# Kernel tuning notes

Measured on AMD Instinct MI355X. Metric: run time of the kernel, lower is better.

## Reference

```python
import jax, jax.numpy as jnp
import numpy as np

TAPS = 5
DELAY = 3
ITERATIONS = 2
EPS = 1e-10


def wpe_one_iteration(Y, power, taps=TAPS, delay=DELAY, eps=EPS):
    """One WPE iteration.
    Y: (B, F, C, T) complex STFT signal.
    power: (B, F, T) real power estimate.
    Returns dereverberated signal, same shape as Y.
    """
    B, F, C, T = Y.shape
    inv_pow = 1.0 / jnp.maximum(power, eps)  # (B,F,T)

    # Tap-delayed (Toeplitz-like) stacked signal: Ytil[..., p, d, t] = Y[..., d, t - delay - p]
    Ytil = jnp.stack(
        [jnp.pad(Y[..., : T - delay - p], ((0, 0), (0, 0), (0, 0), (delay + p, 0)))
         for p in range(taps)],
        axis=2,
    )  # (B, F, taps, C, T)

    # Original implementation only accumulates statistics for frames where the
    # full tap window is available: t >= delay + taps - 1.
    valid = (jnp.arange(T) >= delay + taps - 1).astype(power.dtype)
    w = inv_pow * valid  # (B,F,T)

    Psi_w = jnp.conj(Ytil) * w[:, :, None, None, :]  # (B,F,taps,C,T)

    # Power-weighted covariance matrix R[(p,d),(q,e)] and cross-correlation b[(p,d),e]
    R = jnp.einsum('bfpdt,bfqet->bfpdqe', Psi_w, Ytil).reshape(B, F, taps * C, taps * C)
    b = jnp.einsum('bfpdt,bfet->bfpde', Psi_w, Y).reshape(B, F, taps * C, C)

    eye = jnp.eye(taps * C, dtype=R.dtype)
    # Batched per-frequency linear solve for the conjugate filter matrix
    G_conj = jnp.linalg.solve(R + eps * eye, b).reshape(B, F, taps, C, C)

    # reverb tail: sum over taps p and source channels d
    reverb_tail = jnp.einsum('bfpde,bfpdt->bfet', G_conj, Ytil)
    return Y - reverb_tail


def setup_inputs() -> dict:
    key = jax.random.key(0)
    k1, k2 = jax.random.split(key)
    B, T, C, F = 8, 512, 8, 257
    data_real = jax.random.normal(k1, (B, T, C, F), dtype=jnp.float32)
    data_imag = jax.random.normal(k2, (B, T, C, F), dtype=jnp.float32)
    ilens = jnp.full((B,), T, dtype=jnp.int64)
    return {"data_real": data_real, "data_imag": data_imag, "ilens": ilens}


def reference(data_real, data_imag, ilens):
    # data: (B, T, C, F) -> (B, F, C, T)
    data = (data_real + 1j * data_imag).astype(jnp.complex64)
    Y = jnp.transpose(data, (0, 3, 2, 1))  # (B,F,C,T)
    enhanced = Y
    for _ in range(ITERATIONS):
        power = jnp.mean(enhanced.real ** 2 + enhanced.imag ** 2, axis=-2)  # (B,F,T)
        enhanced = wpe_one_iteration(Y, power)
        # NOTE: original code calls `enhanced.masked_fill(...)` (non in-place),
        # whose result is discarded -> it is a no-op; ilens here are all == T anyway.
    enhanced = jnp.transpose(enhanced, (0, 3, 2, 1))  # (B,T,C,F)
    # Return real/imag stacked so output is a real float tensor (B,T,C,F,2)
    return jnp.stack([enhanced.real, enhanced.imag], axis=-1)
```

## Files before the change

### kernel.cpp

```cpp
#include <hip/hip_runtime.h>

constexpr int BB = 8;
constexpr int TT = 512;
constexpr int CHN = 8;
constexpr int FF = 257;
constexpr int TAPS = 5;
constexpr int DELAY = 3;
constexpr int NBF = BB * FF;
constexpr int ROWQ = 20;
constexpr int MC = 48;
constexpr int RS = 98;

typedef short s8v __attribute__((ext_vector_type(8)));
typedef float f4  __attribute__((ext_vector_type(4)));

__global__ void k_pack(const float* __restrict__ re, const float* __restrict__ im,
                       float* __restrict__ Yg, float* __restrict__ pw) {
  const int ft = blockIdx.x, tt = blockIdx.y, b = blockIdx.z;
  const int f0 = ft * 32, t0 = tt * 16;
  __shared__ float ls[32 * 258];
  const int tid = threadIdx.x;
  const int l = tid & 31;
  const int r = tid >> 5;
  const int f = f0 + l;
  if (f < FF) {
    for (int k = 0; k < 32; ++k) {
      const int task = r + 8 * k;
      const int ri = task & 1;
      const int c  = (task >> 1) & 7;
      const int t  = task >> 4;
      const float* src = ri ? im : re;
      const float v = src[(((size_t)b * TT + t0 + t) * CHN + c) * FF + f];
      ls[l * 258 + (t * 16 + c * 2 + ri)] = v;
    }
  }
  __syncthreads();
  for (int ff = 0; ff < 32; ++ff) {
    const int fg = f0 + ff;
    if (fg >= FF) break;
    Yg[(((size_t)b * FF + fg) * TT + t0) * 16 + tid] = ls[ff * 258 + tid];
  }
  if (f < FF) {
#pragma unroll
    for (int s = 0; s < 2; ++s) {
      const int t = (tid >> 5) + 8 * s;
      const float* row = &ls[l * 258 + t * 16];
      float ss = 0.f;
#pragma unroll
      for (int q = 0; q < 8; ++q) {
        const float2 v = *(const float2*)&row[q * 2];
        ss += v.x * v.x + v.y * v.y;
      }
      pw[((size_t)b * FF + f) * TT + t0 + t] = ss * (1.0f / CHN);
    }
  }
}

__device__ __forceinline__ unsigned bf16rn(float x) {
  unsigned b = __float_as_uint(x);
  return (b + 0x7fffu + ((b >> 16) & 1u)) >> 16;
}

__global__ __launch_bounds__(384, 4)
void k_corr(const float* __restrict__ Yg,
            const float* __restrict__ pw,
            float2* __restrict__ Mg) {
  const int bf = blockIdx.x;
  __shared__ float pre[512 * 9];
  __shared__ float pim[512 * 9];
  __shared__ unsigned short tiles[4 * 1920];
  const int tid = threadIdx.x;

  for (int t = tid; t < TT; t += 384) {
    const float p = pw[(size_t)bf * TT + t];
    pre[t * 9 + 8] = (t >= DELAY + TAPS - 1) ? rsqrtf(fmaxf(p, 1e-10f)) : 0.0f;
  }
  const float4* ybase4 = (const float4*)(Yg + (size_t)bf * TT * 16);
  for (int fi = tid; fi < TT * 4; fi += 384) {
    const int t = fi >> 2, q = fi & 3;
    const float4 v = ybase4[fi];
    pre[t * 9 + 2 * q] = v.x; pre[t * 9 + 2 * q + 1] = v.z;
    pim[t * 9 + 2 * q] = v.y; pim[t * 9 + 2 * q + 1] = v.w;
  }
  __syncthreads();

  const int lane = tid & 63, wv = tid >> 6;
  const int rt = (wv < 3) ? 0 : (wv < 5 ? 1 : 2);
  const int ct = (wv < 3) ? wv : (wv < 5 ? wv - 2 : 2);
  const int lr = lane & 15, lk = lane >> 4;
  const int aoff = (rt * 16 + lr) * 40 + lk * 8;
  const int boff = (ct * 16 + lr) * 40 + lk * 8;

  f4 accre  = {0.f, 0.f, 0.f, 0.f};
  f4 accim1 = {0.f, 0.f, 0.f, 0.f};
  f4 accim2 = {0.f, 0.f, 0.f, 0.f};

  for (int kt = 0; kt < 16; ++kt) {
    const int kt0 = kt * 32;
#pragma unroll
    for (int cc = 0; cc < 2; ++cc) {
      const int c = tid + cc * 384;
      const int kp = c & 15, row = c >> 4;
      const int t = kt0 + 2 * kp;
      const int sh = (row < 40) ? (DELAY + (row >> 3)) : 0;
      const int e  = (row < 40) ? (row & 7) : (row - 40);
      int s0 = t - sh;     if (s0 < 0) s0 = 0;
      int s1 = t + 1 - sh; if (s1 < 0) s1 = 0;
      const float u0 = pre[t * 9 + 8], u1 = pre[(t + 1) * 9 + 8];
      const float v0r = u0 * pre[s0 * 9 + e], v0i = u0 * pim[s0 * 9 + e];
      const float v1r = u1 * pre[s1 * 9 + e], v1i = u1 * pim[s1 * 9 + e];
      const int idx = row * 40 + 2 * kp;
      {
        const unsigned b0 = __float_as_uint(v0r), b1 = __float_as_uint(v1r);
        *(unsigned*)&tiles[idx] = (b0 >> 16) | (b1 & 0xffff0000u);
        *(unsigned*)&tiles[1920 + idx] =
            bf16rn(v0r - __uint_as_float(b0 & 0xffff0000u)) |
            (bf16rn(v1r - __uint_as_float(b1 & 0xffff0000u)) << 16);
      }
      {
        const unsigned b0 = __float_as_uint(v0i), b1 = __float_as_uint(v1i);
        *(unsigned*)&tiles[3840 + idx] = (b0 >> 16) | (b1 & 0xffff0000u);
        *(unsigned*)&tiles[5760 + idx] =
            bf16rn(v0i - __uint_as_float(b0 & 0xffff0000u)) |
            (bf16rn(v1i - __uint_as_float(b1 & 0xffff0000u)) << 16);
      }
    }
    __syncthreads();
    const s8v crhA = *(const s8v*)&tiles[aoff];
    const s8v crlA = *(const s8v*)&tiles[1920 + aoff];
    const s8v cihA = *(const s8v*)&tiles[3840 + aoff];
    const s8v cilA = *(const s8v*)&tiles[5760 + aoff];
    const s8v crhB = *(const s8v*)&tiles[boff];
    const s8v crlB = *(const s8v*)&tiles[1920 + boff];
    const s8v cihB = *(const s8v*)&tiles[3840 + boff];
    const s8v cilB = *(const s8v*)&tiles[5760 + boff];
    accre  = __builtin_amdgcn_mfma_f32_16x16x32_bf16(crhA, crhB, accre, 0, 0, 0);
    accre  = __builtin_amdgcn_mfma_f32_16x16x32_bf16(crlA, crhB, accre, 0, 0, 0);
    accre  = __builtin_amdgcn_mfma_f32_16x16x32_bf16(crhA, crlB, accre, 0, 0, 0);
    accre  = __builtin_amdgcn_mfma_f32_16x16x32_bf16(cihA, cihB, accre, 0, 0, 0);
    accre  = __builtin_amdgcn_mfma_f32_16x16x32_bf16(cilA, cihB, accre, 0, 0, 0);
    accre  = __builtin_amdgcn_mfma_f32_16x16x32_bf16(cihA, cilB, accre, 0, 0, 0);
    accim1 = __builtin_amdgcn_mfma_f32_16x16x32_bf16(crhA, cihB, accim1, 0, 0, 0);
    accim1 = __builtin_amdgcn_mfma_f32_16x16x32_bf16(crlA, cihB, accim1, 0, 0, 0);
    accim1 = __builtin_amdgcn_mfma_f32_16x16x32_bf16(crhA, cilB, accim1, 0, 0, 0);
    accim2 = __builtin_amdgcn_mfma_f32_16x16x32_bf16(cihA, crhB, accim2, 0, 0, 0);
    accim2 = __builtin_amdgcn_mfma_f32_16x16x32_bf16(cilA, crhB, accim2, 0, 0, 0);
    accim2 = __builtin_amdgcn_mfma_f32_16x16x32_bf16(cihA, crlB, accim2, 0, 0, 0);
    __syncthreads();
  }

#pragma unroll
  for (int r = 0; r < 4; ++r) {
    const int i = rt * 16 + lk * 4 + r;
    const int j = ct * 16 + lr;
    const float revl = accre[r];
    const float imvl = accim1[r] - accim2[r];
    if (i < 40) {
      float rr = revl;
      if (i == j) rr += 1e-10f;
      Mg[((size_t)bf * 40 + i) * MC + j] = make_float2(rr, imvl);
    }
    if (rt < ct && j < 40) {
      Mg[((size_t)bf * 40 + j) * MC + i] = make_float2(revl, -imvl);
    }
  }
}

__global__ __launch_bounds__(128) void k_solve(const float2* __restrict__ Mg,
                                               float2* __restrict__ Gg) {
  const int bf = blockIdx.x;
  __shared__ float ml[40 * RS];
  const int tid = threadIdx.x;
  for (int idx = tid; idx < 40 * MC; idx += 128) {
    const int i = idx / MC, j = idx - i * MC;
    float2 v = Mg[((size_t)bf * 40 + i) * MC + j];
    *(float2*)&ml[i * RS + j * 2] = v;
  }
  __syncthreads();
  const int li = tid >> 3, lj = tid & 7;
  for (int k = 0; k < 40; ++k) {
    const float2 pv = *(float2*)&ml[k * RS + k * 2];
    const float den = pv.x * pv.x + pv.y * pv.y;
    const float inr = pv.x / den, ini = -pv.y / den;
    for (int i = k + 1 + li; i < 40; i += 16) {
      const float2 aik = *(float2*)&ml[i * RS + k * 2];
      const float fr = aik.x * inr - aik.y * ini;
      const float fi = aik.x * ini + aik.y * inr;
      for (int j = k + 1 + lj; j < MC; j += 8) {
        const float2 ak = *(float2*)&ml[k * RS + j * 2];
        float2 ai = *(float2*)&ml[i * RS + j * 2];
        ai.x -= fr * ak.x - fi * ak.y;
        ai.y -= fr * ak.y + fi * ak.x;
        *(float2*)&ml[i * RS + j * 2] = ai;
      }
    }
    __syncthreads();
  }
  const int lane = tid & 63, wave = tid >> 6;
  const int e = 4 * wave + (lane & 3), cc = lane >> 2;
  for (int k = 39; k >= 0; --k) {
    float sr = 0.f, si = 0.f;
    for (int j = k + 1 + cc; j < 40; j += 16) {
      const float2 u = *(float2*)&ml[k * RS + j * 2];
      const float2 x = *(float2*)&ml[j * RS + (40 + e) * 2];
      sr += u.x * x.x - u.y * x.y;
      si += u.x * x.y + u.y * x.x;
    }
    sr += __shfl_xor(sr, 4);  si += __shfl_xor(si, 4);
    sr += __shfl_xor(sr, 8);  si += __shfl_xor(si, 8);
    sr += __shfl_xor(sr, 16); si += __shfl_xor(si, 16);
    sr += __shfl_xor(sr, 32); si += __shfl_xor(si, 32);
    if (cc == 0) {
      const float2 pvt = *(float2*)&ml[k * RS + k * 2];
      const float den = pvt.x * pvt.x + pvt.y * pvt.y;
      const float inr = pvt.x / den, ini = -pvt.y / den;
      const float2 rhs = *(float2*)&ml[k * RS + (40 + e) * 2];
      const float nr = rhs.x - sr, ni = rhs.y - si;
      *(float2*)&ml[k * RS + (40 + e) * 2] =
          make_float2(nr * inr - ni * ini, nr * ini + ni * inr);
    }
    asm volatile("" ::: "memory");
  }
  __syncthreads();
  for (int idx = tid; idx < 320; idx += 128) {
    const int i = idx >> 3, ee = idx & 7;
    Gg[(size_t)bf * 320 + idx] = *(float2*)&ml[i * RS + (40 + ee) * 2];
  }
}

template <int MODE>
__global__ __launch_bounds__(256) void k_tail(float* __restrict__ Yg,
                                              const float2* __restrict__ Gg,
                                              float* __restrict__ pw) {
  const int bf = blockIdx.x;
  __shared__ float yl[TT * ROWQ];
  __shared__ float gl[640];
  const int tid = threadIdx.x;
  for (int idx = tid; idx < 320; idx += 256) {
    float2 g = Gg[(size_t)bf * 320 + idx];
    *(float2*)&gl[idx * 2] = g;
  }
  const float4* ybase4 = (const float4*)(Yg + (size_t)bf * TT * 16);
  for (int fi = tid; fi < TT * 4; fi += 256) {
    const int row = fi >> 2, wq = fi & 3;
    *((float4*)&yl[row * ROWQ + wq * 4]) = ybase4[fi];
  }
  __syncthreads();

  const int t0 = tid;
  const int t1 = tid + 256;
  float acc[2][16];
  {
    const float* yr0 = &yl[t0 * ROWQ];
    const float* yr1 = &yl[t1 * ROWQ];
#pragma unroll
    for (int q = 0; q < 16; ++q) { acc[0][q] = yr0[q]; acc[1][q] = yr1[q]; }
  }
#pragma unroll 1
  for (int p = 0; p < TAPS; ++p) {
    const int rp0 = t0 - DELAY - p;
    const int rp1 = t1 - DELAY - p;
    const float* yrow0 = &yl[(rp0 >= 0 ? rp0 : 0) * ROWQ];
    const float* yrow1 = &yl[rp1 * ROWQ];
    const float m0 = (rp0 >= 0) ? 1.0f : 0.0f;
    const float* gp = &gl[p * 128];
#pragma unroll
    for (int d = 0; d < CHN; ++d) {
      const float y0r = m0 * yrow0[2 * d], y0i = m0 * yrow0[2 * d + 1];
      const float y1r = yrow1[2 * d],      y1i = yrow1[2 * d + 1];
      const float4 g0 = *(const float4*)&gp[d * 16 + 0];
      const float4 g1 = *(const float4*)&gp[d * 16 + 4];
      const float4 g2 = *(const float4*)&gp[d * 16 + 8];
      const float4 g3 = *(const float4*)&gp[d * 16 + 12];
      const float gr[8] = {g0.x, g0.z, g1.x, g1.z, g2.x, g2.z, g3.x, g3.z};
      const float gi[8] = {g0.y, g0.w, g1.y, g1.w, g2.y, g2.w, g3.y, g3.w};
#pragma unroll
      for (int ee = 0; ee < 8; ++ee) {
        acc[0][2 * ee]     -= gr[ee] * y0r - gi[ee] * y0i;
        acc[0][2 * ee + 1] -= gr[ee] * y0i + gi[ee] * y0r;
        acc[1][2 * ee]     -= gr[ee] * y1r - gi[ee] * y1i;
        acc[1][2 * ee + 1] -= gr[ee] * y1i + gi[ee] * y1r;
      }
    }
  }
  float* ybase = Yg + (size_t)bf * TT * 16;
  if (MODE == 0) {
#pragma unroll
    for (int s = 0; s < 2; ++s) {
      const int t = tid + s * 256;
      float ss = 0.f;
#pragma unroll
      for (int q = 0; q < 16; ++q) ss += acc[s][q] * acc[s][q];
      pw[(size_t)bf * TT + t] = ss * (1.0f / CHN);
    }
  } else {
#pragma unroll
    for (int s = 0; s < 2; ++s) {
      const int t = tid + s * 256;
      float4* dst = (float4*)(ybase + (size_t)t * 16);
      dst[0] = make_float4(acc[s][0], acc[s][1], acc[s][2], acc[s][3]);
      dst[1] = make_float4(acc[s][4], acc[s][5], acc[s][6], acc[s][7]);
      dst[2] = make_float4(acc[s][8], acc[s][9], acc[s][10], acc[s][11]);
      dst[3] = make_float4(acc[s][12], acc[s][13], acc[s][14], acc[s][15]);
    }
  }
}

__global__ void k_unpack(const float* __restrict__ Yg, float* __restrict__ out) {
  const int ft = blockIdx.x, tt = blockIdx.y, b = blockIdx.z;
  const int f0 = ft * 32, t0 = tt * 16;
  __shared__ float ls[32 * 258];
  const int tid = threadIdx.x;
  for (int ff = 0; ff < 32; ++ff) {
    const int fg = f0 + ff;
    if (fg >= FF) break;
    ls[ff * 258 + tid] = Yg[(((size_t)b * FF + fg) * TT + t0) * 16 + tid];
  }
  __syncthreads();
  const int l = tid & 31, r = tid >> 5;
  const int fg = f0 + l;
  if (fg < FF) {
    for (int k = 0; k < 16; ++k) {
      const int task = r + 8 * k;
      const int t = task >> 3, c = task & 7;
      const float2 v = *(float2*)&ls[l * 258 + t * 16 + c * 2];
      *(float2*)&out[((((size_t)b * TT + t0 + t) * CHN + c) * FF + fg) * 2] = v;
    }
  }
}

extern "C" void kernel_launch(void* const* d_in, const int* in_sizes, int n_in,
                              void* d_out, int out_size, void* d_ws, size_t ws_size,
                              hipStream_t stream) {
  const float* re = (const float*)d_in[0];
  const float* im = (const float*)d_in[1];
  float* ws = (float*)d_ws;

  float*  Yg = ws;
  float*  pw = Yg + (size_t)NBF * TT * 16;
  float2* Mg = (float2*)(pw + (size_t)NBF * TT);
  float2* Gg = Mg + (size_t)NBF * 40 * MC;
  float*  out = (float*)d_out;

  const dim3 gridT(9, 32, BB);
  k_pack<<<gridT, 256, 0, stream>>>(re, im, Yg, pw);

  for (int iter = 0; iter < 2; ++iter) {
    k_corr<<<NBF, 384, 0, stream>>>(Yg, pw, Mg);
    k_solve<<<NBF, 128, 0, stream>>>(Mg, Gg);
    if (iter == 0)
      k_tail<0><<<NBF, 256, 0, stream>>>(Yg, Gg, pw);
    else
      k_tail<1><<<NBF, 256, 0, stream>>>(Yg, Gg, pw);
  }

  k_unpack<<<gridT, 256, 0, stream>>>(Yg, out);
}
```

Measured before the change: 507.8 us.

## Fuse correlation and linear solve into one kernel sharing LDS matrix

Merges the covariance kernel and the per-frequency complex Gaussian elimination into one kernel. The covariance result is written straight into shared memory, aliased over the bf16 tile buffer, so it no longer goes through global memory. This drops a launch and the global write/read of the 40x48 matrix. The solve now runs with 384 threads, one row per thread group in elimination, and only two waves do back substitution. LDS use per block rises, which may lower occupancy of the correlation phase.

After: 659.5 us. 29.9% more time.

```diff
diff --git a/kernel.cpp b/kernel.cpp
--- a/kernel.cpp
+++ b/kernel.cpp
@@ -62,13 +62,14 @@
 }
 
 __global__ __launch_bounds__(384, 4)
-void k_corr(const float* __restrict__ Yg,
-            const float* __restrict__ pw,
-            float2* __restrict__ Mg) {
+void k_corrsolve(const float* __restrict__ Yg,
+                 const float* __restrict__ pw,
+                 float2* __restrict__ Gg) {
   const int bf = blockIdx.x;
   __shared__ float pre[512 * 9];
   __shared__ float pim[512 * 9];
-  __shared__ unsigned short tiles[4 * 1920];
+  __shared__ __align__(16) float ml[40 * RS];
+  unsigned short* tiles = (unsigned short*)ml;
   const int tid = threadIdx.x;
 
   for (int t = tid; t < TT; t += 384) {
@@ -158,31 +159,21 @@
     if (i < 40) {
       float rr = revl;
       if (i == j) rr += 1e-10f;
-      Mg[((size_t)bf * 40 + i) * MC + j] = make_float2(rr, imvl);
+      ml[i * RS + j * 2] = rr; ml[i * RS + j * 2 + 1] = imvl;
     }
     if (rt < ct && j < 40) {
-      Mg[((size_t)bf * 40 + j) * MC + i] = make_float2(revl, -imvl);
-    }
-  }
-}
-
-__global__ __launch_bounds__(128) void k_solve(const float2* __restrict__ Mg,
-                                               float2* __restrict__ Gg) {
-  const int bf = blockIdx.x;
-  __shared__ float ml[40 * RS];
-  const int tid = threadIdx.x;
-  for (int idx = tid; idx < 40 * MC; idx += 128) {
-    const int i = idx / MC, j = idx - i * MC;
-    float2 v = Mg[((size_t)bf * 40 + i) * MC + j];
-    *(float2*)&ml[i * RS + j * 2] = v;
-  }
-  __syncthreads();
+      ml[j * RS + i * 2] = revl; ml[j * RS + i * 2 + 1] = -imvl;
+    }
+  }
+  __syncthreads();
+
   const int li = tid >> 3, lj = tid & 7;
   for (int k = 0; k < 40; ++k) {
     const float2 pv = *(float2*)&ml[k * RS + k * 2];
     const float den = pv.x * pv.x + pv.y * pv.y;
     const float inr = pv.x / den, ini = -pv.y / den;
-    for (int i = k + 1 + li; i < 40; i += 16) {
+    const int i = k + 1 + li;
+    if (i < 40) {
       const float2 aik = *(float2*)&ml[i * RS + k * 2];
       const float fr = aik.x * inr - aik.y * ini;
       const float fi = aik.x * ini + aik.y * inr;
@@ -196,33 +187,35 @@
     }
     __syncthreads();
   }
-  const int lane = tid & 63, wave = tid >> 6;
-  const int e = 4 * wave + (lane & 3), cc = lane >> 2;
-  for (int k = 39; k >= 0; --k) {
-    float sr = 0.f, si = 0.f;
-    for (int j = k + 1 + cc; j < 40; j += 16) {
-      const float2 u = *(float2*)&ml[k * RS + j * 2];
-      const float2 x = *(float2*)&ml[j * RS + (40 + e) * 2];
-      sr += u.x * x.x - u.y * x.y;
-      si += u.x * x.y + u.y * x.x;
-    }
-    sr += __shfl_xor(sr, 4);  si += __shfl_xor(si, 4);
-    sr += __shfl_xor(sr, 8);  si += __shfl_xor(si, 8);
-    sr += __shfl_xor(sr, 16); si += __shfl_xor(si, 16);
-    sr += __shfl_xor(sr, 32); si += __shfl_xor(si, 32);
-    if (cc == 0) {
-      const float2 pvt = *(float2*)&ml[k * RS + k * 2];
-      const float den = pvt.x * pvt.x + pvt.y * pvt.y;
-      const float inr = pvt.x / den, ini = -pvt.y / den;
-      const float2 rhs = *(float2*)&ml[k * RS + (40 + e) * 2];
-      const float nr = rhs.x - sr, ni = rhs.y - si;
-      *(float2*)&ml[k * RS + (40 + e) * 2] =
-          make_float2(nr * inr - ni * ini, nr * ini + ni * inr);
-    }
-    asm volatile("" ::: "memory");
-  }
-  __syncthreads();
-  for (int idx = tid; idx < 320; idx += 128) {
+
+  if (wv < 2) {
+    const int e = 4 * wv + (lane & 3), cc = lane >> 2;
+    for (int k = 39; k >= 0; --k) {
+      float sr = 0.f, si = 0.f;
+      for (int j = k + 1 + cc; j < 40; j += 16) {
+        const float2 u = *(float2*)&ml[k * RS + j * 2];
+        const float2 x = *(float2*)&ml[j * RS + (40 + e) * 2];
+        sr += u.x * x.x - u.y * x.y;
+        si += u.x * x.y + u.y * x.x;
+      }
+      sr += __shfl_xor(sr, 4);  si += __shfl_xor(si, 4);
+      sr += __shfl_xor(sr, 8);  si += __shfl_xor(si, 8);
+      sr += __shfl_xor(sr, 16); si += __shfl_xor(si, 16);
+      sr += __shfl_xor(sr, 32); si += __shfl_xor(si, 32);
+      if (cc == 0) {
+        const float2 pvt = *(float2*)&ml[k * RS + k * 2];
+        const float den = pvt.x * pvt.x + pvt.y * pvt.y;
+        const float inr = pvt.x / den, ini = -pvt.y / den;
+        const float2 rhs = *(float2*)&ml[k * RS + (40 + e) * 2];
+        const float nr = rhs.x - sr, ni = rhs.y - si;
+        *(float2*)&ml[k * RS + (40 + e) * 2] =
+            make_float2(nr * inr - ni * ini, nr * ini + ni * inr);
+      }
+      asm volatile("" ::: "memory");
+    }
+  }
+  __syncthreads();
+  for (int idx = tid; idx < 320; idx += 384) {
     const int i = idx >> 3, ee = idx & 7;
     Gg[(size_t)bf * 320 + idx] = *(float2*)&ml[i * RS + (40 + ee) * 2];
   }
@@ -338,16 +331,14 @@
 
   float*  Yg = ws;
   float*  pw = Yg + (size_t)NBF * TT * 16;
-  float2* Mg = (float2*)(pw + (size_t)NBF * TT);
-  float2* Gg = Mg + (size_t)NBF * 40 * MC;
+  float2* Gg = (float2*)(pw + (size_t)NBF * TT);
   float*  out = (float*)d_out;
 
   const dim3 gridT(9, 32, BB);
   k_pack<<<gridT, 256, 0, stream>>>(re, im, Yg, pw);
 
   for (int iter = 0; iter < 2; ++iter) {
-    k_corr<<<NBF, 384, 0, stream>>>(Yg, pw, Mg);
-    k_solve<<<NBF, 128, 0, stream>>>(Mg, Gg);
+    k_corrsolve<<<NBF, 384, 0, stream>>>(Yg, pw, Gg);
     if (iter == 0)
       k_tail<0><<<NBF, 256, 0, stream>>>(Yg, Gg, pw);
     else
```
